# Kernel tuning notes

Measured on AMD Instinct MI355X. Metric: run time of the kernel, lower is better.

Reference implementation:

```python
import jax, jax.numpy as jnp
import numpy as np

N_NODES = 100000
N_EDGES = 1600000
NFEAT, NHID, NCLASS = 512, 128, 64


def setup_inputs() -> dict:
    key = jax.random.key(0)
    ks = jax.random.split(key, 8)
    y = jax.random.normal(ks[0], (N_NODES, NFEAT), dtype=jnp.float32)
    src = jax.random.randint(ks[1], (N_EDGES,), 0, N_NODES, dtype=jnp.int64)
    dst = jax.random.randint(ks[2], (N_EDGES,), 0, N_NODES, dtype=jnp.int64)
    edge_w = jax.random.uniform(ks[3], (N_EDGES,), dtype=jnp.float32)
    # GraphConvolution params (Glorot-ish scale)
    W1 = jax.random.normal(ks[4], (NFEAT, NHID), dtype=jnp.float32) / np.sqrt(NFEAT)
    b1 = jax.random.normal(ks[5], (NHID,), dtype=jnp.float32) * 0.01
    W2 = jax.random.normal(ks[6], (NHID, NCLASS), dtype=jnp.float32) / np.sqrt(NHID)
    b2 = jax.random.normal(ks[7], (NCLASS,), dtype=jnp.float32) * 0.01
    return {"y": y, "src": src, "dst": dst, "edge_w": edge_w,
            "W1": W1, "b1": b1, "W2": W2, "b2": b2}


def _graph_conv(x, W, b, src, dst, edge_w, n_nodes):
    # support = x @ W ; out = spmm(adj, support) + b  (adj in COO form)
    support = x @ W                                   # [N, out_dim]
    msgs = support[src] * edge_w[:, None]             # [E, out_dim] gather
    agg = jax.ops.segment_sum(msgs, dst, num_segments=n_nodes)  # scatter-add
    return agg + b


def reference(y, src, dst, edge_w, W1, b1, W2, b2):
    h = jax.nn.leaky_relu(_graph_conv(y, W1, b1, src, dst, edge_w, N_NODES),
                          negative_slope=0.01)        # F.leaky_relu default
    y_embedding = h
    logits = _graph_conv(h, W2, b2, src, dst, edge_w, N_NODES)
    return (jax.nn.softmax(logits, axis=1), y_embedding)
```

## Files before the change

### kernel.cpp

```cpp
#include <hip/hip_runtime.h>
#include <hip/hip_fp16.h>

#define NN 100000
#define NE 1600000
#define F0 512
#define F1 128
#define F2 64

typedef short bf16x8 __attribute__((ext_vector_type(8)));
typedef float f32x4  __attribute__((ext_vector_type(4)));

static __device__ __forceinline__ unsigned short f2bf(float f) {
    unsigned int u = __float_as_uint(f);
    return (unsigned short)((u + 0x7FFFu + ((u >> 16) & 1u)) >> 16);
}

static __device__ __forceinline__ unsigned short f2h(float f) {
    __half h = __float2half(f);
    return *(unsigned short*)&h;
}

static __device__ __forceinline__ float2 h2f2(unsigned int u) {
    __half2 h = *(__half2*)&u;
    return __half22float2(h);
}

__global__ __launch_bounds__(256)
void wt_kernel(const float* __restrict__ W1, const float* __restrict__ W2,
               unsigned short* __restrict__ W1t, unsigned short* __restrict__ W2t)
{
    int i = blockIdx.x * 256 + threadIdx.x;
    if (i < F0 * F1) {
        int n = i / F0, k = i % F0;
        W1t[i] = f2bf(W1[k * F1 + n]);
    } else {
        int j = i - F0 * F1;
        if (j < F1 * F2) {
            int n = j / F1, k = j % F1;
            W2t[j] = f2bf(W2[k * F2 + n]);
        }
    }
}

template<int BM, int BN, int BK, int TN, bool FILL>
__global__ __launch_bounds__(256)
void gemm_edge_kernel(const float* __restrict__ A, const unsigned short* __restrict__ Bt,
                      unsigned short* __restrict__ C, int M, int K, int N,
                      int row_base, int gemm_blocks,
                      const int* __restrict__ src, const int* __restrict__ dst,
                      const float* __restrict__ ew, const int* __restrict__ rowptr,
                      int* __restrict__ cnt, int* __restrict__ rank,
                      int2* __restrict__ rec, int ne)
{
    constexpr int LDA = BK + 8;
    constexpr int LDB = BK + 8;
    __shared__ unsigned short As[BM * LDA];
    __shared__ unsigned short Bs[BN * LDB];

    if ((int)blockIdx.x >= gemm_blocks) {
        int e = ((int)blockIdx.x - gemm_blocks) * 256 + threadIdx.x;
        if (e < ne) {
            if constexpr (!FILL) {
                rank[e] = atomicAdd(&cnt[dst[e]], 1);
            } else {
                int d = dst[e];
                int pos = rowptr[d] + rank[e];
                rec[pos] = make_int2(src[e], __float_as_int(ew[e]));
            }
        }
        return;
    }

    const int tid  = threadIdx.x;
    const int wave = tid >> 6;
    const int lane = tid & 63;
    const int lr   = lane & 15;
    const int quad = lane >> 4;
    const int row0 = row_base + (int)blockIdx.x * BM;

    f32x4 acc[2][TN];
#pragma unroll
    for (int i = 0; i < 2; i++)
#pragma unroll
        for (int j = 0; j < TN; j++) acc[i][j] = (f32x4)0.f;

    for (int k0 = 0; k0 < K; k0 += BK) {
#pragma unroll
        for (int l = tid; l < BM * (BK / 4); l += 256) {
            int m  = l / (BK / 4);
            int kq = l % (BK / 4);
            int rg = row0 + m; if (rg >= M) rg = M - 1;
            float4 v = *(const float4*)(A + (long long)rg * K + k0 + kq * 4);
            ushort4 b = make_ushort4(f2bf(v.x), f2bf(v.y), f2bf(v.z), f2bf(v.w));
            *(ushort4*)(&As[m * LDA + kq * 4]) = b;
        }
#pragma unroll
        for (int l = tid; l < BN * (BK / 8); l += 256) {
            int n  = l / (BK / 8);
            int ko = l % (BK / 8);
            uint4 v = *(const uint4*)(Bt + (long long)n * K + k0 + ko * 8);
            *(uint4*)(&Bs[n * LDB + ko * 8]) = v;
        }
        __syncthreads();

#pragma unroll
        for (int kk = 0; kk < BK; kk += 32) {
            bf16x8 a[2], b[TN];
#pragma unroll
            for (int tm = 0; tm < 2; tm++)
                a[tm] = *(const bf16x8*)(&As[(wave * 32 + tm * 16 + lr) * LDA + kk + quad * 8]);
#pragma unroll
            for (int tn = 0; tn < TN; tn++)
                b[tn] = *(const bf16x8*)(&Bs[(tn * 16 + lr) * LDB + kk + quad * 8]);
#pragma unroll
            for (int tm = 0; tm < 2; tm++)
#pragma unroll
                for (int tn = 0; tn < TN; tn++)
                    acc[tm][tn] = __builtin_amdgcn_mfma_f32_16x16x32_bf16(
                        a[tm], b[tn], acc[tm][tn], 0, 0, 0);
        }
        __syncthreads();
    }

#pragma unroll
    for (int tm = 0; tm < 2; tm++) {
#pragma unroll
        for (int r = 0; r < 4; r++) {
            int row = row0 + wave * 32 + tm * 16 + quad * 4 + r;
            if (row < M) {
#pragma unroll
                for (int tn = 0; tn < TN; tn++)
                    C[(long long)row * N + tn * 16 + lr] = f2h(acc[tm][tn][r]);
            }
        }
    }
}

__global__ __launch_bounds__(256)
void scan1_kernel(const int* __restrict__ cnt, int* __restrict__ rowptr,
                  int* __restrict__ bsum, int n)
{
    __shared__ int s[256];
    int t = threadIdx.x;
    int i = blockIdx.x * 256 + t;
    int v = (i < n) ? cnt[i] : 0;
    s[t] = v;
    __syncthreads();
#pragma unroll
    for (int off = 1; off < 256; off <<= 1) {
        int x = (t >= off) ? s[t - off] : 0;
        __syncthreads();
        s[t] += x;
        __syncthreads();
    }
    if (i < n) rowptr[i] = s[t] - v;
    if (t == 255) bsum[blockIdx.x] = s[255];
}

__global__ __launch_bounds__(512)
void scan2_kernel(int* __restrict__ bsum, int nb, int* __restrict__ rowptr, int n, int ne)
{
    __shared__ int s[512];
    int t = threadIdx.x;
    int v = (t < nb) ? bsum[t] : 0;
    s[t] = v;
    __syncthreads();
#pragma unroll
    for (int off = 1; off < 512; off <<= 1) {
        int x = (t >= off) ? s[t - off] : 0;
        __syncthreads();
        s[t] += x;
        __syncthreads();
    }
    if (t < nb) bsum[t] = s[t] - v;
    if (t == 0) rowptr[n] = ne;
}

__global__ __launch_bounds__(256)
void scan3_kernel(int* __restrict__ rowptr, const int* __restrict__ bsum, int n)
{
    int i = blockIdx.x * 256 + threadIdx.x;
    if (i < n) rowptr[i] += bsum[i >> 8];
}

__global__ __launch_bounds__(256)
void agg1_fused_kernel(const unsigned int* __restrict__ sup, const int2* __restrict__ rec,
                       const int* __restrict__ rowptr, const float2* __restrict__ b1,
                       const unsigned short* __restrict__ W2t,
                       float2* __restrict__ h, unsigned short* __restrict__ sup2, int n)
{
    constexpr int LDH = F1 + 8;
    __shared__ unsigned short hsb[16 * LDH];

    const int tid  = threadIdx.x;
    const int w    = tid >> 6;
    const int lane = tid & 63;
    const int base = blockIdx.x * 16;

    float2 bb = b1[lane];

#pragma unroll
    for (int i = 0; i < 4; i++) {
        int row  = w * 4 + i;
        int node = base + row;
        float2 acc = make_float2(0.f, 0.f);
        if (node < n) {
            int j   = rowptr[node];
            int end = rowptr[node + 1];
            for (; j + 8 <= end; j += 8) {
                int2 r[8];
#pragma unroll
                for (int u = 0; u < 8; u++) r[u] = rec[j + u];
                unsigned int uu[8];
#pragma unroll
                for (int u = 0; u < 8; u++)
                    uu[u] = sup[(long long)r[u].x * 64 + lane];
#pragma unroll
                for (int u = 0; u < 8; u++) {
                    float2 f = h2f2(uu[u]);
                    float  ww = __int_as_float(r[u].y);
                    acc.x = fmaf(f.x, ww, acc.x);
                    acc.y = fmaf(f.y, ww, acc.y);
                }
            }
            for (; j + 2 <= end; j += 2) {
                int2 r0 = rec[j];
                int2 r1 = rec[j + 1];
                unsigned int u0 = sup[(long long)r0.x * 64 + lane];
                unsigned int u1 = sup[(long long)r1.x * 64 + lane];
                float2 f0 = h2f2(u0);
                float2 f1 = h2f2(u1);
                float w0 = __int_as_float(r0.y);
                float w1 = __int_as_float(r1.y);
                acc.x = fmaf(f0.x, w0, acc.x);  acc.y = fmaf(f0.y, w0, acc.y);
                acc.x = fmaf(f1.x, w1, acc.x);  acc.y = fmaf(f1.y, w1, acc.y);
            }
            if (j < end) {
                int2 r0 = rec[j];
                unsigned int u0 = sup[(long long)r0.x * 64 + lane];
                float2 f0 = h2f2(u0);
                float w0 = __int_as_float(r0.y);
                acc.x = fmaf(f0.x, w0, acc.x);
                acc.y = fmaf(f0.y, w0, acc.y);
            }
            acc.x += bb.x;
            acc.y += bb.y;
            acc.x = acc.x > 0.f ? acc.x : 0.01f * acc.x;
            acc.y = acc.y > 0.f ? acc.y : 0.01f * acc.y;
            h[(long long)node * 64 + lane] = acc;
        }
        ushort2 hv = (node < n) ? make_ushort2(f2bf(acc.x), f2bf(acc.y))
                                : make_ushort2(0, 0);
        *(ushort2*)(&hsb[row * LDH + lane * 2]) = hv;
    }
    __syncthreads();

    const int lr   = lane & 15;
    const int quad = lane >> 4;
    f32x4 acc2 = (f32x4)0.f;
#pragma unroll
    for (int kk = 0; kk < F1; kk += 32) {
        bf16x8 a = *(const bf16x8*)(&hsb[lr * LDH + kk + quad * 8]);
        bf16x8 b = *(const bf16x8*)(W2t + (w * 16 + lr) * F1 + kk + quad * 8);
        acc2 = __builtin_amdgcn_mfma_f32_16x16x32_bf16(a, b, acc2, 0, 0, 0);
    }
#pragma unroll
    for (int r = 0; r < 4; r++) {
        int node = base + quad * 4 + r;
        if (node < n)
            sup2[(long long)node * 64 + w * 16 + lr] = f2h(acc2[r]);
    }
}

__global__ __launch_bounds__(256)
void agg2_kernel(const unsigned short* __restrict__ sup, const int2* __restrict__ rec,
                 const int* __restrict__ rowptr, const float* __restrict__ b2,
                 float* __restrict__ out, int n)
{
    int node = blockIdx.x * 4 + (threadIdx.x >> 6);
    int lane = threadIdx.x & 63;
    if (node >= n) return;

    int j   = rowptr[node];
    int end = rowptr[node + 1];
    float acc = 0.f;

    for (; j + 8 <= end; j += 8) {
        int2 r[8];
#pragma unroll
        for (int u = 0; u < 8; u++) r[u] = rec[j + u];
        unsigned short uu[8];
#pragma unroll
        for (int u = 0; u < 8; u++)
            uu[u] = sup[(long long)r[u].x * 64 + lane];
#pragma unroll
        for (int u = 0; u < 8; u++)
            acc = fmaf(__half2float(*(__half*)&uu[u]), __int_as_float(r[u].y), acc);
    }
    for (; j + 2 <= end; j += 2) {
        int2 r0 = rec[j];
        int2 r1 = rec[j + 1];
        unsigned short u0 = sup[(long long)r0.x * 64 + lane];
        unsigned short u1 = sup[(long long)r1.x * 64 + lane];
        acc = fmaf(__half2float(*(__half*)&u0), __int_as_float(r0.y), acc);
        acc = fmaf(__half2float(*(__half*)&u1), __int_as_float(r1.y), acc);
    }
    if (j < end) {
        int2 r0 = rec[j];
        unsigned short u0 = sup[(long long)r0.x * 64 + lane];
        acc = fmaf(__half2float(*(__half*)&u0), __int_as_float(r0.y), acc);
    }

    float v = acc + b2[lane];
    float m = v;
#pragma unroll
    for (int off = 32; off; off >>= 1) m = fmaxf(m, __shfl_xor(m, off, 64));
    float e = __expf(v - m);
    float s = e;
#pragma unroll
    for (int off = 32; off; off >>= 1) s += __shfl_xor(s, off, 64);
    out[(long long)node * 64 + lane] = e / s;
}

extern "C" void kernel_launch(void* const* d_in, const int* in_sizes, int n_in,
                              void* d_out, int out_size, void* d_ws, size_t ws_size,
                              hipStream_t stream)
{
    const float* y   = (const float*)d_in[0];
    const int*   src = (const int*)  d_in[1];
    const int*   dst = (const int*)  d_in[2];
    const float* ew  = (const float*)d_in[3];
    const float* W1  = (const float*)d_in[4];
    const float* b1  = (const float*)d_in[5];
    const float* W2  = (const float*)d_in[6];
    const float* b2  = (const float*)d_in[7];

    float* out     = (float*)d_out;
    float* softout = out;
    float* h       = out + (size_t)NN * F2;

    char* ws = (char*)d_ws;
    size_t o = 0;
    auto alloc = [&](size_t bytes) -> void* {
        void* p = ws + o;
        o = (o + bytes + 255) & ~(size_t)255;
        return p;
    };
    unsigned short* sup  = (unsigned short*)alloc((size_t)NN * F1 * 2);
    unsigned short* sup2 = (unsigned short*)alloc((size_t)NN * F2 * 2);
    int2*           rec  = (int2*)          alloc((size_t)NE * 8);
    int*            rank = (int*)           alloc((size_t)NE * 4);
    int*            rowptr = (int*)         alloc((size_t)(NN + 2) * 4);
    int*            cnt  = (int*)           alloc((size_t)NN * 4);
    int*            bsum = (int*)           alloc(512 * 4);
    unsigned short* W1t  = (unsigned short*)alloc((size_t)F0 * F1 * 2);
    unsigned short* W2t  = (unsigned short*)alloc((size_t)F1 * F2 * 2);

    const int NB = (NN + 255) / 256;
    const int GB = (NN + 127) / 128;
    const int GA = GB / 2;
    const int EB = (NE + 255) / 256;

    hipMemsetAsync(cnt, 0, (size_t)NN * 4, stream);
    wt_kernel<<<(F0 * F1 + F1 * F2 + 255) / 256, 256, 0, stream>>>(W1, W2, W1t, W2t);

    gemm_edge_kernel<128, 128, 64, 8, false><<<GA + EB, 256, 0, stream>>>(
        y, W1t, sup, NN, F0, F1, 0, GA,
        src, dst, ew, rowptr, cnt, rank, rec, NE);

    scan1_kernel<<<NB, 256, 0, stream>>>(cnt, rowptr, bsum, NN);
    scan2_kernel<<<1, 512, 0, stream>>>(bsum, NB, rowptr, NN, NE);
    scan3_kernel<<<NB, 256, 0, stream>>>(rowptr, bsum, NN);

    gemm_edge_kernel<128, 128, 64, 8, true><<<(GB - GA) + EB, 256, 0, stream>>>(
        y, W1t, sup, NN, F0, F1, GA * 128, GB - GA,
        src, dst, ew, rowptr, cnt, rank, rec, NE);

    agg1_fused_kernel<<<(NN + 15) / 16, 256, 0, stream>>>(
        (const unsigned int*)sup, rec, rowptr, (const float2*)b1, W2t,
        (float2*)h, sup2, NN);

    agg2_kernel<<<(NN + 3) / 4, 256, 0, stream>>>(
        sup2, rec, rowptr, b2, softout, NN);
}
```

Measured before the change: 570.9 us.

## Fold memset and scan3 into neighbors, widen per-lane gathers in aggregation kernels

The cnt memset now runs inside the weight-transpose kernel, and the scan3 kernel is removed: consumers add the block offset bsum[d>>8] themselves, with scan1 extending to index n so rowptr[n] comes out correctly. Both aggregation kernels now use half-waves per node with wider per-lane loads (uint2/uint, float4/float2 stores), so each wave processes two nodes at once. The GEMM split point is fixed at 312 blocks instead of half of the row blocks. Together these cut kernel launches and per-lane memory instructions, at the cost of an extra bsum lookup on every rowptr read.

New measurement: 553.2 us. 3.1% less time.

```diff
diff --git a/kernel.cpp b/kernel.cpp
--- a/kernel.cpp
+++ b/kernel.cpp
@@ -27,7 +27,8 @@
 
 __global__ __launch_bounds__(256)
 void wt_kernel(const float* __restrict__ W1, const float* __restrict__ W2,
-               unsigned short* __restrict__ W1t, unsigned short* __restrict__ W2t)
+               unsigned short* __restrict__ W1t, unsigned short* __restrict__ W2t,
+               int* __restrict__ cnt, int grid_threads)
 {
     int i = blockIdx.x * 256 + threadIdx.x;
     if (i < F0 * F1) {
@@ -40,6 +41,7 @@
             W2t[j] = f2bf(W2[k * F2 + n]);
         }
     }
+    for (int z = i; z < NN + 256; z += grid_threads) cnt[z] = 0;
 }
 
 template<int BM, int BN, int BK, int TN, bool FILL>
@@ -49,6 +51,7 @@
                       int row_base, int gemm_blocks,
                       const int* __restrict__ src, const int* __restrict__ dst,
                       const float* __restrict__ ew, const int* __restrict__ rowptr,
+                      const int* __restrict__ bsum,
                       int* __restrict__ cnt, int* __restrict__ rank,
                       int2* __restrict__ rec, int ne)
 {
@@ -64,7 +67,7 @@
                 rank[e] = atomicAdd(&cnt[dst[e]], 1);
             } else {
                 int d = dst[e];
-                int pos = rowptr[d] + rank[e];
+                int pos = rowptr[d] + bsum[d >> 8] + rank[e];
                 rec[pos] = make_int2(src[e], __float_as_int(ew[e]));
             }
         }
@@ -143,7 +146,7 @@
     __shared__ int s[256];
     int t = threadIdx.x;
     int i = blockIdx.x * 256 + t;
-    int v = (i < n) ? cnt[i] : 0;
+    int v = (i <= n) ? cnt[i] : 0;
     s[t] = v;
     __syncthreads();
 #pragma unroll
@@ -153,12 +156,12 @@
         s[t] += x;
         __syncthreads();
     }
-    if (i < n) rowptr[i] = s[t] - v;
+    if (i <= n) rowptr[i] = s[t] - v;
     if (t == 255) bsum[blockIdx.x] = s[255];
 }
 
 __global__ __launch_bounds__(512)
-void scan2_kernel(int* __restrict__ bsum, int nb, int* __restrict__ rowptr, int n, int ne)
+void scan2_kernel(int* __restrict__ bsum, int nb)
 {
     __shared__ int s[512];
     int t = threadIdx.x;
@@ -173,21 +176,14 @@
         __syncthreads();
     }
     if (t < nb) bsum[t] = s[t] - v;
-    if (t == 0) rowptr[n] = ne;
-}
-
-__global__ __launch_bounds__(256)
-void scan3_kernel(int* __restrict__ rowptr, const int* __restrict__ bsum, int n)
-{
-    int i = blockIdx.x * 256 + threadIdx.x;
-    if (i < n) rowptr[i] += bsum[i >> 8];
 }
 
 __global__ __launch_bounds__(256)
 void agg1_fused_kernel(const unsigned int* __restrict__ sup, const int2* __restrict__ rec,
-                       const int* __restrict__ rowptr, const float2* __restrict__ b1,
+                       const int* __restrict__ rowptr, const int* __restrict__ bsum,
+                       const float* __restrict__ b1,
                        const unsigned short* __restrict__ W2t,
-                       float2* __restrict__ h, unsigned short* __restrict__ sup2, int n)
+                       float* __restrict__ h, unsigned short* __restrict__ sup2, int n)
 {
     constexpr int LDH = F1 + 8;
     __shared__ unsigned short hsb[16 * LDH];
@@ -195,63 +191,61 @@
     const int tid  = threadIdx.x;
     const int w    = tid >> 6;
     const int lane = tid & 63;
+    const int half = lane >> 5;
+    const int sl   = lane & 31;
     const int base = blockIdx.x * 16;
 
-    float2 bb = b1[lane];
-
-#pragma unroll
-    for (int i = 0; i < 4; i++) {
-        int row  = w * 4 + i;
+    float4 bb = *(const float4*)(b1 + sl * 4);
+
+#pragma unroll
+    for (int it = 0; it < 2; it++) {
+        int row  = w * 4 + it * 2 + half;
         int node = base + row;
-        float2 acc = make_float2(0.f, 0.f);
+        float4 acc = make_float4(0.f, 0.f, 0.f, 0.f);
         if (node < n) {
-            int j   = rowptr[node];
-            int end = rowptr[node + 1];
+            int j   = rowptr[node]     + bsum[node >> 8];
+            int end = rowptr[node + 1] + bsum[(node + 1) >> 8];
             for (; j + 8 <= end; j += 8) {
                 int2 r[8];
 #pragma unroll
                 for (int u = 0; u < 8; u++) r[u] = rec[j + u];
-                unsigned int uu[8];
+                uint2 uu[8];
 #pragma unroll
                 for (int u = 0; u < 8; u++)
-                    uu[u] = sup[(long long)r[u].x * 64 + lane];
+                    uu[u] = *(const uint2*)(&sup[(long long)r[u].x * 64 + sl * 2]);
 #pragma unroll
                 for (int u = 0; u < 8; u++) {
-                    float2 f = h2f2(uu[u]);
+                    float2 fa = h2f2(uu[u].x);
+                    float2 fb = h2f2(uu[u].y);
                     float  ww = __int_as_float(r[u].y);
-                    acc.x = fmaf(f.x, ww, acc.x);
-                    acc.y = fmaf(f.y, ww, acc.y);
+                    acc.x = fmaf(fa.x, ww, acc.x);
+                    acc.y = fmaf(fa.y, ww, acc.y);
+                    acc.z = fmaf(fb.x, ww, acc.z);
+                    acc.w = fmaf(fb.y, ww, acc.w);
                 }
             }
-            for (; j + 2 <= end; j += 2) {
+            for (; j < end; j++) {
                 int2 r0 = rec[j];
-                int2 r1 = rec[j + 1];
-                unsigned int u0 = sup[(long long)r0.x * 64 + lane];
-                unsigned int u1 = sup[(long long)r1.x * 64 + lane];
-                float2 f0 = h2f2(u0);
-                float2 f1 = h2f2(u1);
-                float w0 = __int_as_float(r0.y);
-                float w1 = __int_as_float(r1.y);
-                acc.x = fmaf(f0.x, w0, acc.x);  acc.y = fmaf(f0.y, w0, acc.y);
-                acc.x = fmaf(f1.x, w1, acc.x);  acc.y = fmaf(f1.y, w1, acc.y);
+                uint2 u0 = *(const uint2*)(&sup[(long long)r0.x * 64 + sl * 2]);
+                float2 fa = h2f2(u0.x);
+                float2 fb = h2f2(u0.y);
+                float  ww = __int_as_float(r0.y);
+                acc.x = fmaf(fa.x, ww, acc.x);
+                acc.y = fmaf(fa.y, ww, acc.y);
+                acc.z = fmaf(fb.x, ww, acc.z);
+                acc.w = fmaf(fb.y, ww, acc.w);
             }
-            if (j < end) {
-                int2 r0 = rec[j];
-                unsigned int u0 = sup[(long long)r0.x * 64 + lane];
-                float2 f0 = h2f2(u0);
-                float w0 = __int_as_float(r0.y);
-                acc.x = fmaf(f0.x, w0, acc.x);
-                acc.y = fmaf(f0.y, w0, acc.y);
-            }
-            acc.x += bb.x;
-            acc.y += bb.y;
+            acc.x += bb.x;  acc.y += bb.y;  acc.z += bb.z;  acc.w += bb.w;
             acc.x = acc.x > 0.f ? acc.x : 0.01f * acc.x;
             acc.y = acc.y > 0.f ? acc.y : 0.01f * acc.y;
-            h[(long long)node * 64 + lane] = acc;
-        }
-        ushort2 hv = (node < n) ? make_ushort2(f2bf(acc.x), f2bf(acc.y))
-                                : make_ushort2(0, 0);
-        *(ushort2*)(&hsb[row * LDH + lane * 2]) = hv;
+            acc.z = acc.z > 0.f ? acc.z : 0.01f * acc.z;
+            acc.w = acc.w > 0.f ? acc.w : 0.01f * acc.w;
+            *(float4*)(h + (long long)node * 128 + sl * 4) = acc;
+        }
+        ushort4 hv = (node < n)
+            ? make_ushort4(f2bf(acc.x), f2bf(acc.y), f2bf(acc.z), f2bf(acc.w))
+            : make_ushort4(0, 0, 0, 0);
+        *(ushort4*)(&hsb[row * LDH + sl * 4]) = hv;
     }
     __syncthreads();
 
@@ -274,52 +268,55 @@
 
 __global__ __launch_bounds__(256)
 void agg2_kernel(const unsigned short* __restrict__ sup, const int2* __restrict__ rec,
-                 const int* __restrict__ rowptr, const float* __restrict__ b2,
-                 float* __restrict__ out, int n)
-{
-    int node = blockIdx.x * 4 + (threadIdx.x >> 6);
-    int lane = threadIdx.x & 63;
+                 const int* __restrict__ rowptr, const int* __restrict__ bsum,
+                 const float* __restrict__ b2, float* __restrict__ out, int n)
+{
+    const int lane = threadIdx.x & 63;
+    const int half = lane >> 5;
+    const int sl   = lane & 31;
+    const int node = blockIdx.x * 8 + (threadIdx.x >> 6) * 2 + half;
     if (node >= n) return;
 
-    int j   = rowptr[node];
-    int end = rowptr[node + 1];
-    float acc = 0.f;
+    int j   = rowptr[node]     + bsum[node >> 8];
+    int end = rowptr[node + 1] + bsum[(node + 1) >> 8];
+    float2 acc = make_float2(0.f, 0.f);
 
     for (; j + 8 <= end; j += 8) {
         int2 r[8];
 #pragma unroll
         for (int u = 0; u < 8; u++) r[u] = rec[j + u];
-        unsigned short uu[8];
+        unsigned int uu[8];
 #pragma unroll
         for (int u = 0; u < 8; u++)
-            uu[u] = sup[(long long)r[u].x * 64 + lane];
-#pragma unroll
-        for (int u = 0; u < 8; u++)
-            acc = fmaf(__half2float(*(__half*)&uu[u]), __int_as_float(r[u].y), acc);
-    }
-    for (; j + 2 <= end; j += 2) {
+            uu[u] = *(const unsigned int*)(&sup[(long long)r[u].x * 64 + sl * 2]);
+#pragma unroll
+        for (int u = 0; u < 8; u++) {
+            float2 f = h2f2(uu[u]);
+            float  ww = __int_as_float(r[u].y);
+            acc.x = fmaf(f.x, ww, acc.x);
+            acc.y = fmaf(f.y, ww, acc.y);
+        }
+    }
+    for (; j < end; j++) {
         int2 r0 = rec[j];
-        int2 r1 = rec[j + 1];
-        unsigned short u0 = sup[(long long)r0.x * 64 + lane];
-        unsigned short u1 = sup[(long long)r1.x * 64 + lane];
-        acc = fmaf(__half2float(*(__half*)&u0), __int_as_float(r0.y), acc);
-        acc = fmaf(__half2float(*(__half*)&u1), __int_as_float(r1.y), acc);
-    }
-    if (j < end) {
-        int2 r0 = rec[j];
-        unsigned short u0 = sup[(long long)r0.x * 64 + lane];
-        acc = fmaf(__half2float(*(__half*)&u0), __int_as_float(r0.y), acc);
-    }
-
-    float v = acc + b2[lane];
-    float m = v;
-#pragma unroll
-    for (int off = 32; off; off >>= 1) m = fmaxf(m, __shfl_xor(m, off, 64));
-    float e = __expf(v - m);
-    float s = e;
-#pragma unroll
-    for (int off = 32; off; off >>= 1) s += __shfl_xor(s, off, 64);
-    out[(long long)node * 64 + lane] = e / s;
+        unsigned int u0 = *(const unsigned int*)(&sup[(long long)r0.x * 64 + sl * 2]);
+        float2 f = h2f2(u0);
+        float  ww = __int_as_float(r0.y);
+        acc.x = fmaf(f.x, ww, acc.x);
+        acc.y = fmaf(f.y, ww, acc.y);
+    }
+
+    float2 bv = *(const float2*)(b2 + sl * 2);
+    float2 v  = make_float2(acc.x + bv.x, acc.y + bv.y);
+    float m = fmaxf(v.x, v.y);
+#pragma unroll
+    for (int off = 16; off; off >>= 1) m = fmaxf(m, __shfl_xor(m, off, 64));
+    float2 e = make_float2(__expf(v.x - m), __expf(v.y - m));
+    float s = e.x + e.y;
+#pragma unroll
+    for (int off = 16; off; off >>= 1) s += __shfl_xor(s, off, 64);
+    float inv = 1.f / s;
+    *(float2*)(out + (long long)node * 64 + sl * 2) = make_float2(e.x * inv, e.y * inv);
 }
 
 extern "C" void kernel_launch(void* const* d_in, const int* in_sizes, int n_in,
@@ -351,35 +348,32 @@
     int2*           rec  = (int2*)          alloc((size_t)NE * 8);
     int*            rank = (int*)           alloc((size_t)NE * 4);
     int*            rowptr = (int*)         alloc((size_t)(NN + 2) * 4);
-    int*            cnt  = (int*)           alloc((size_t)NN * 4);
+    int*            cnt  = (int*)           alloc((size_t)(NN + 256) * 4);
     int*            bsum = (int*)           alloc(512 * 4);
     unsigned short* W1t  = (unsigned short*)alloc((size_t)F0 * F1 * 2);
     unsigned short* W2t  = (unsigned short*)alloc((size_t)F1 * F2 * 2);
 
     const int NB = (NN + 255) / 256;
     const int GB = (NN + 127) / 128;
-    const int GA = GB / 2;
+    const int GA = 312;
     const int EB = (NE + 255) / 256;
 
-    hipMemsetAsync(cnt, 0, (size_t)NN * 4, stream);
-    wt_kernel<<<(F0 * F1 + F1 * F2 + 255) / 256, 256, 0, stream>>>(W1, W2, W1t, W2t);
+    wt_kernel<<<NB, 256, 0, stream>>>(W1, W2, W1t, W2t, cnt, NB * 256);
 
     gemm_edge_kernel<128, 128, 64, 8, false><<<GA + EB, 256, 0, stream>>>(
         y, W1t, sup, NN, F0, F1, 0, GA,
-        src, dst, ew, rowptr, cnt, rank, rec, NE);
+        src, dst, ew, rowptr, bsum, cnt, rank, rec, NE);
 
     scan1_kernel<<<NB, 256, 0, stream>>>(cnt, rowptr, bsum, NN);
-    scan2_kernel<<<1, 512, 0, stream>>>(bsum, NB, rowptr, NN, NE);
-    scan3_kernel<<<NB, 256, 0, stream>>>(rowptr, bsum, NN);
+    scan2_kernel<<<1, 512, 0, stream>>>(bsum, NB);
 
     gemm_edge_kernel<128, 128, 64, 8, true><<<(GB - GA) + EB, 256, 0, stream>>>(
         y, W1t, sup, NN, F0, F1, GA * 128, GB - GA,
-        src, dst, ew, rowptr, cnt, rank, rec, NE);
+        src, dst, ew, rowptr, bsum, cnt, rank, rec, NE);
 
     agg1_fused_kernel<<<(NN + 15) / 16, 256, 0, stream>>>(
-        (const unsigned int*)sup, rec, rowptr, (const float2*)b1, W2t,
-        (float2*)h, sup2, NN);
-
-    agg2_kernel<<<(NN + 3) / 4, 256, 0, stream>>>(
-        sup2, rec, rowptr, b2, softout, NN);
-}
+        (const unsigned int*)sup, rec, rowptr, bsum, b1, W2t, h, sup2, NN);
+
+    agg2_kernel<<<(NN + 7) / 8, 256, 0, stream>>>(
+        sup2, rec, rowptr, bsum, b2, softout, NN);
+}
```
